# Performance work log

Hardware: AMD Instinct MI355X
Metric: run time of the kernel (lower is better)

## Reference

```python
import jax, jax.numpy as jnp
import numpy as np

B, T, D, H = 2, 2048, 1024, 16
HD = D // H
SCALE = HD ** -0.5
NEG_INF = float(np.finfo(np.float32).min)


def setup_inputs() -> dict:
    key = jax.random.key(0)
    ks = jax.random.split(key, 10)
    s = 1.0 / np.sqrt(D)
    x = jax.random.normal(ks[0], (B, T, D), dtype=jnp.float32)
    # causal mask, True = keep, shape (B,1,T,T)
    mask = jnp.broadcast_to(jnp.tril(jnp.ones((T, T), dtype=bool)), (B, 1, T, T))
    Wq = jax.random.normal(ks[1], (D, D), dtype=jnp.float32) * s
    bq = jax.random.normal(ks[2], (D,), dtype=jnp.float32) * s
    Wk = jax.random.normal(ks[3], (D, D), dtype=jnp.float32) * s
    bk = jax.random.normal(ks[4], (D,), dtype=jnp.float32) * s
    Wv = jax.random.normal(ks[5], (D, D), dtype=jnp.float32) * s
    bv = jax.random.normal(ks[6], (D,), dtype=jnp.float32) * s
    Wo = jax.random.normal(ks[7], (D, D), dtype=jnp.float32) * s
    bo = jax.random.normal(ks[8], (D,), dtype=jnp.float32) * s
    return {"x": x, "mask": mask, "Wq": Wq, "bq": bq, "Wk": Wk, "bk": bk,
            "Wv": Wv, "bv": bv, "Wo": Wo, "bo": bo}


def _split_heads(t):
    # (B,T,D) -> (B,H,T,HD)
    return t.reshape(B, T, H, HD).transpose(0, 2, 1, 3)


def masked_rowwise_softmax(scores, mask):
    # mask: bool, True = keep; fully-masked rows return zeros.
    s = scores.astype(jnp.float32)
    masked = jnp.where(mask, s, NEG_INF)
    row_max = jnp.max(masked, axis=-1, keepdims=True)
    exps = jnp.exp(masked - row_max) * mask.astype(jnp.float32)
    denom = jnp.maximum(jnp.sum(exps, axis=-1, keepdims=True), 1e-12)
    return (exps / denom).astype(scores.dtype)


def reference(x, mask, Wq, bq, Wk, bk, Wv, bv, Wo, bo):
    q = _split_heads(x @ Wq.T + bq)
    k = _split_heads(x @ Wk.T + bk)
    v = _split_heads(x @ Wv.T + bv)
    scores = jnp.einsum('bhqd,bhkd->bhqk', q, k) * SCALE
    m = jnp.broadcast_to(mask, (B, H, T, T))
    attn = masked_rowwise_softmax(scores, m)
    y = jnp.einsum('bhqk,bhkd->bhqd', attn, v)
    y = y.transpose(0, 2, 1, 3).reshape(B, T, D)
    return y @ Wo.T + bo
```

## Files before the change

### kernel.cpp

```cpp
#include <hip/hip_runtime.h>

#define B_ 2
#define H_ 16
#define T_ 2048
#define D_ 1024
#define HD_ 64
#define NEG_HUGE (-3.402823466e38f)
#define QSCALE 0.18033688011112042f

typedef unsigned short u16;
typedef unsigned int u32;
typedef __attribute__((ext_vector_type(8))) short bf16x8;
typedef __attribute__((ext_vector_type(4))) float f32x4;
typedef __attribute__((ext_vector_type(4))) u32 u32x4;

typedef const __attribute__((address_space(1))) void* gas_t;
typedef __attribute__((address_space(3))) void* las_t;

__device__ __forceinline__ u16 f2bf(float f) {
    u32 u = __builtin_bit_cast(u32, f);
    u += 0x7FFFu + ((u >> 16) & 1u);
    return (u16)(u >> 16);
}

__device__ __forceinline__ u32 pk2bf(float f0, float f1) {
    const u32 a0 = __builtin_bit_cast(u32, f0) + 0x8000u;
    const u32 a1 = __builtin_bit_cast(u32, f1) + 0x8000u;
    return __builtin_amdgcn_perm(a1, a0, 0x07060302u);
}

__device__ __forceinline__ uint2 pk4bf(f32x4 a) {
    uint2 r;
    r.x = pk2bf(a[0], a[1]);
    r.y = pk2bf(a[2], a[3]);
    return r;
}

__device__ __forceinline__ f32x4 mfma16(bf16x8 a, bf16x8 b, f32x4 c) {
    return __builtin_amdgcn_mfma_f32_16x16x32_bf16(a, b, c, 0, 0, 0);
}

__global__ __launch_bounds__(256) void to_bf16(
    const float* __restrict__ x,  const float* __restrict__ wq,
    const float* __restrict__ wk, const float* __restrict__ wv,
    const float* __restrict__ wo, u16* __restrict__ dst)
{
    const size_t g = ((size_t)blockIdx.x * 256 + threadIdx.x) * 8;
    const float* src; size_t off;
    if      (g < (size_t)(4u << 20)) { src = x;  off = g; }
    else if (g < (size_t)(5u << 20)) { src = wq; off = g - (size_t)(4u << 20); }
    else if (g < (size_t)(6u << 20)) { src = wk; off = g - (size_t)(5u << 20); }
    else if (g < (size_t)(7u << 20)) { src = wv; off = g - (size_t)(6u << 20); }
    else                             { src = wo; off = g - (size_t)(7u << 20); }
    const float4 a = *(const float4*)&src[off];
    const float4 b = *(const float4*)&src[off + 4];
    ushort4 lo = make_ushort4(f2bf(a.x), f2bf(a.y), f2bf(a.z), f2bf(a.w));
    ushort4 hi = make_ushort4(f2bf(b.x), f2bf(b.y), f2bf(b.z), f2bf(b.w));
    *(ushort4*)&dst[g]     = lo;
    *(ushort4*)&dst[g + 4] = hi;
}

__device__ __forceinline__ void gemm128_core(
    const u16* __restrict__ P0, const u16* __restrict__ P1,
    const int m0, const int n0, u16* As, u16* Bs, f32x4 (&acc)[4][4])
{
    const int tid  = threadIdx.x;
    const int lane = tid & 63;
    const int quad = lane >> 4;
    const int l15  = lane & 15;
    const int w    = tid >> 6;
    const int wm   = (w >> 1) << 6;
    const int wn   = (w & 1) << 6;
    const int swz  = l15 & 7;

    size_t aoff[4], boff[4];
    int    loff[4];
#pragma unroll
    for (int i = 0; i < 4; ++i) {
        const int slot = i * 256 + tid;
        const int r = slot >> 3, c = slot & 7;
        const int gc = (c ^ (r & 7)) << 3;
        aoff[i] = (size_t)(m0 + r) * D_ + gc;
        boff[i] = (size_t)(n0 + r) * D_ + gc;
        loff[i] = slot * 8;
    }
    int rowA[4], rowB[4];
#pragma unroll
    for (int i = 0; i < 4; ++i) {
        rowA[i] = (wm + i * 16 + l15) * 64;
        rowB[i] = (wn + i * 16 + l15) * 64;
    }

    bf16x8 pa[4], pb[4];
#pragma unroll
    for (int i = 0; i < 4; ++i) {
        pa[i] = *(const bf16x8*)&P0[aoff[i]];
        pb[i] = *(const bf16x8*)&P1[boff[i]];
    }

    for (int k0 = 0; k0 < D_; k0 += 64) {
        __syncthreads();
#pragma unroll
        for (int i = 0; i < 4; ++i) {
            *(bf16x8*)&As[loff[i]] = pa[i];
            *(bf16x8*)&Bs[loff[i]] = pb[i];
        }
        if (k0 + 64 < D_) {
            const int kn = k0 + 64;
#pragma unroll
            for (int i = 0; i < 4; ++i) {
                pa[i] = *(const bf16x8*)&P0[aoff[i] + kn];
                pb[i] = *(const bf16x8*)&P1[boff[i] + kn];
            }
        }
        __syncthreads();
#pragma unroll
        for (int s = 0; s < 2; ++s) {
            const int ch = (((s << 2) + quad) ^ swz) << 3;
            bf16x8 am[4], bm[4];
#pragma unroll
            for (int mi = 0; mi < 4; ++mi) am[mi] = *(const bf16x8*)&As[rowA[mi] + ch];
#pragma unroll
            for (int ni = 0; ni < 4; ++ni) bm[ni] = *(const bf16x8*)&Bs[rowB[ni] + ch];
#pragma unroll
            for (int mi = 0; mi < 4; ++mi)
#pragma unroll
                for (int ni = 0; ni < 4; ++ni)
                    acc[mi][ni] = mfma16(am[mi], bm[ni], acc[mi][ni]);
        }
    }
}

__global__ __launch_bounds__(512, 2) void gemm_qkv(
    const u16* __restrict__ xb,
    const u16* __restrict__ Wqb, const u16* __restrict__ Wkb, const u16* __restrict__ Wvb,
    const float* __restrict__ bq, const float* __restrict__ bk, const float* __restrict__ bv,
    u16* __restrict__ Qb, u16* __restrict__ Kb, u16* __restrict__ Vtb)
{
    __shared__ u16 lds[65536];
    const int tid  = threadIdx.x;
    const int lane = tid & 63;
    const int quad = lane >> 4;
    const int l15  = lane & 15;
    const int w    = tid >> 6;
    const int wr   = w >> 2;
    const int wc   = w & 3;
    const int swz7 = l15 & 7;

    const int L  = blockIdx.x;
    const int wg = (L & 7) * 24 + (L >> 3);
    const int ftile = wg >> 4;
    const int ttile = wg & 15;
    const int z  = ftile >> 2;
    const int fb = (ftile & 3) << 8;

    const u16* PA; const u16* PB;
    int Ra, Rb;
    if (z == 0)      { PA = Wqb; PB = xb;  Ra = fb;         Rb = ttile << 8; }
    else if (z == 1) { PA = Wkb; PB = xb;  Ra = fb;         Rb = ttile << 8; }
    else             { PA = xb;  PB = Wvb; Ra = ttile << 8; Rb = fb;         }

    const int rr  = tid >> 3;
    const int cc8 = ((tid & 7) ^ (rr & 7)) << 3;
    size_t srcA[4], srcB[4];
#pragma unroll
    for (int i = 0; i < 4; ++i) {
        srcA[i] = (size_t)(Ra + i * 64 + rr) * D_ + cc8;
        srcB[i] = (size_t)(Rb + i * 64 + rr) * D_ + cc8;
    }
    const int dstT = tid * 8;

#define QKV_STAGE(p, kt) do {                                               \
    const size_t ko_ = (size_t)(kt) * 64;                                   \
    _Pragma("unroll")                                                       \
    for (int i_ = 0; i_ < 4; ++i_)                                          \
        __builtin_amdgcn_global_load_lds((gas_t)(PA + srcA[i_] + ko_),      \
            (las_t)&lds[((p) << 14) + i_ * 4096 + dstT], 16, 0, 0);         \
    _Pragma("unroll")                                                       \
    for (int i_ = 0; i_ < 4; ++i_)                                          \
        __builtin_amdgcn_global_load_lds((gas_t)(PB + srcB[i_] + ko_),      \
            (las_t)&lds[32768 + ((p) << 14) + i_ * 4096 + dstT], 16, 0, 0); \
} while (0)

    const int baseA = ((wr << 7) + l15) * 64;
    const int baseB = 32768 + ((wc << 6) + l15) * 64;
    const int cs0 = (quad ^ swz7) << 3;
    const int cs1 = ((quad + 4) ^ swz7) << 3;

    f32x4 acc[8][4];
#pragma unroll
    for (int i = 0; i < 8; ++i)
#pragma unroll
        for (int j = 0; j < 4; ++j) acc[i][j] = (f32x4){0.f, 0.f, 0.f, 0.f};

    QKV_STAGE(0, 0);
    QKV_STAGE(1, 1);
    asm volatile("s_waitcnt vmcnt(8)" ::: "memory");
    __builtin_amdgcn_s_barrier();

    for (int kt = 0; kt < 16; ++kt) {
        const int pO = (kt & 1) << 14;
        bf16x8 bfr[4][2], afr[4][2];
#pragma unroll
        for (int ni = 0; ni < 4; ++ni) {
            bfr[ni][0] = *(const bf16x8*)&lds[pO + baseB + ni * 1024 + cs0];
            bfr[ni][1] = *(const bf16x8*)&lds[pO + baseB + ni * 1024 + cs1];
        }
#pragma unroll
        for (int mi = 0; mi < 4; ++mi) {
            afr[mi][0] = *(const bf16x8*)&lds[pO + baseA + mi * 1024 + cs0];
            afr[mi][1] = *(const bf16x8*)&lds[pO + baseA + mi * 1024 + cs1];
        }
        __builtin_amdgcn_s_setprio(1);
#pragma unroll
        for (int mi = 0; mi < 4; ++mi)
#pragma unroll
            for (int ni = 0; ni < 4; ++ni) {
                acc[mi][ni] = mfma16(afr[mi][0], bfr[ni][0], acc[mi][ni]);
                acc[mi][ni] = mfma16(afr[mi][1], bfr[ni][1], acc[mi][ni]);
            }
        __builtin_amdgcn_s_setprio(0);
#pragma unroll
        for (int mi = 0; mi < 4; ++mi) {
            afr[mi][0] = *(const bf16x8*)&lds[pO + baseA + (mi + 4) * 1024 + cs0];
            afr[mi][1] = *(const bf16x8*)&lds[pO + baseA + (mi + 4) * 1024 + cs1];
        }
        asm volatile("s_waitcnt lgkmcnt(0)" ::: "memory");
        __builtin_amdgcn_sched_barrier(0);
        __builtin_amdgcn_s_barrier();
        __builtin_amdgcn_sched_barrier(0);
        if (kt + 2 < 16) QKV_STAGE(kt & 1, kt + 2);
        __builtin_amdgcn_s_setprio(1);
#pragma unroll
        for (int mi = 0; mi < 4; ++mi)
#pragma unroll
            for (int ni = 0; ni < 4; ++ni) {
                acc[mi + 4][ni] = mfma16(afr[mi][0], bfr[ni][0], acc[mi + 4][ni]);
                acc[mi + 4][ni] = mfma16(afr[mi][1], bfr[ni][1], acc[mi + 4][ni]);
            }
        __builtin_amdgcn_s_setprio(0);
        if (kt < 14) asm volatile("s_waitcnt vmcnt(8)" ::: "memory");
        else         asm volatile("s_waitcnt vmcnt(0)" ::: "memory");
        __builtin_amdgcn_sched_barrier(0);
        __builtin_amdgcn_s_barrier();
    }
#undef QKV_STAGE

    __syncthreads();
    u16* scr = &lds[w * 8192];
    const int pq   = quad >> 1;
    const int psub = (quad & 1) << 2;

    if (z < 2) {
        const float* bias = (z == 0) ? bq : bk;
        const float  CF   = (z == 0) ? QSCALE : 1.f;
        u16*         Cq   = (z == 0) ? Qb : Kb;
        const int fbw = fb + (wr << 7);
        const int tbw = (ttile << 8) + (wc << 6);
#pragma unroll
        for (int mi = 0; mi < 8; ++mi) {
            const float4 bi = *(const float4*)&bias[fbw + mi * 16 + (quad << 2)];
            const int c = (mi << 1) + pq;
#pragma unroll
            for (int ni = 0; ni < 4; ++ni) {
                const int tl = ni * 16 + l15;
                f32x4 a = acc[mi][ni];
                f32x4 v = { (a[0] + bi.x) * CF, (a[1] + bi.y) * CF,
                            (a[2] + bi.z) * CF, (a[3] + bi.w) * CF };
                *(uint2*)&scr[tl * 128 + ((c ^ (tl & 15)) << 3) + psub] = pk4bf(v);
            }
        }
        __asm__ volatile("s_waitcnt lgkmcnt(0)" ::: "memory");
        const int hb = fbw >> 6;
#pragma unroll
        for (int e = 0; e < 16; ++e) {
            const int tl = (e << 2) + (lane >> 4);
            const int c  = lane & 15;
            bf16x8 v = *(const bf16x8*)&scr[tl * 128 + ((c ^ (tl & 15)) << 3)];
            const int tg = tbw + tl;
            const int bb = tg >> 11, t0 = tg & 2047;
            *(bf16x8*)&Cq[((size_t)((bb << 4) + hb + (c >> 3)) * T_ + t0) * HD_ +
                          ((c & 7) << 3)] = v;
        }
    } else {
        const int fvw = fb + (wc << 6);
        const int h   = fvw >> 6;
        const int tbw = (ttile << 8) + (wr << 7);
#pragma unroll
        for (int ni = 0; ni < 4; ++ni) {
            const int hdrow = ni * 16 + l15;
            const float bi = bv[fvw + ni * 16 + l15];
            const int sw = hdrow & 15;
#pragma unroll
            for (int mi = 0; mi < 8; ++mi) {
                f32x4 a = acc[mi][ni];
                f32x4 v = { a[0] + bi, a[1] + bi, a[2] + bi, a[3] + bi };
                const int c = (mi << 1) + pq;
                *(uint2*)&scr[hdrow * 128 + ((c ^ sw) << 3) + psub] = pk4bf(v);
            }
        }
        __asm__ volatile("s_waitcnt lgkmcnt(0)" ::: "memory");
#pragma unroll
        for (int e = 0; e < 16; ++e) {
            const int hdl = (e << 2) + (lane >> 4);
            const int c   = lane & 15;
            bf16x8 v = *(const bf16x8*)&scr[hdl * 128 + ((c ^ (hdl & 15)) << 3)];
            const int tg = tbw + (c << 3);
            const int bb = tg >> 11, t0 = tg & 2047;
            *(bf16x8*)&Vtb[((size_t)((bb << 4) + h) * HD_ + hdl) * T_ + t0] = v;
        }
    }
}

__global__ __launch_bounds__(256) void gemm_out(
    const u16* __restrict__ Ab, const u16* __restrict__ Wob,
    const float* __restrict__ bo, float* __restrict__ C)
{
    __shared__ u16 As[128 * 64];
    __shared__ u16 Bs[128 * 64];
    const int L   = blockIdx.x;
    const int xcd = L & 7;
    const int kk  = L >> 3;
    const int tt  = (xcd << 2) + (kk & 3);
    const int ft  = kk >> 2;
    const int m0  = tt << 7;
    const int n0  = ft << 7;

    f32x4 acc[4][4];
#pragma unroll
    for (int i = 0; i < 4; ++i)
#pragma unroll
        for (int j = 0; j < 4; ++j) acc[i][j] = (f32x4){0.f, 0.f, 0.f, 0.f};

    gemm128_core(Ab, Wob, m0, n0, As, Bs, acc);

    const int tid  = threadIdx.x;
    const int lane = tid & 63;
    const int quad = lane >> 4;
    const int l15  = lane & 15;
    const int w    = tid >> 6;
    const int wm   = (w >> 1) << 6;
    const int wn   = (w & 1) << 6;

    float bi[4];
#pragma unroll
    for (int ni = 0; ni < 4; ++ni) bi[ni] = bo[n0 + wn + ni * 16 + l15];

#pragma unroll
    for (int mi = 0; mi < 4; ++mi) {
        const int m = m0 + wm + mi * 16 + (quad << 2);
#pragma unroll
        for (int r = 0; r < 4; ++r)
#pragma unroll
            for (int ni = 0; ni < 4; ++ni)
                C[(size_t)(m + r) * D_ + n0 + wn + ni * 16 + l15] = acc[mi][ni][r] + bi[ni];
    }
}

__global__ __launch_bounds__(256) void attn_mfma(
    const u16* __restrict__ Qg, const u16* __restrict__ Kg,
    const u16* __restrict__ Vtg, u16* __restrict__ Out)
{
    __shared__ u16 Ks[128 * 64];
    __shared__ u16 Vs[64 * 128];
    const int tid  = threadIdx.x;
    const int w    = tid >> 6;
    const int lane = tid & 63;
    const int quad = lane >> 4;
    const int l15  = lane & 15;
    const int bh   = blockIdx.x;
    const int qt   = 31 - (int)blockIdx.y;
    const size_t base = (size_t)bh * (T_ * HD_);

    int lK[4], lV[4];
    size_t gK[4], gV[4];
#pragma unroll
    for (int i = 0; i < 4; ++i) {
        const int slot = i * 256 + tid;
        const int rk = slot >> 3, ck = slot & 7;
        lK[i] = rk * 64 + ((ck ^ (rk & 7)) << 3);
        gK[i] = base + (size_t)rk * HD_ + ck * 8;
        const int rv = slot >> 4, cv = slot & 15;
        lV[i] = rv * 128 + ((cv ^ (rv & 15)) << 3);
        gV[i] = base + (size_t)rv * T_ + cv * 8;
    }

    bf16x8 ones;
#pragma unroll
    for (int i = 0; i < 8; ++i) ones[i] = (short)0x3F80;

    const int swz7 = l15 & 7;
    const int b = bh >> 4, h = bh & 15;

    const int qloc = (w << 4) + l15;
    const int qrow = (qt << 6) + qloc;
    const bf16x8 qf0 = *(const bf16x8*)&Qg[base + (size_t)qrow * HD_ + quad * 8];
    const bf16x8 qf1 = *(const bf16x8*)&Qg[base + (size_t)qrow * HD_ + 32 + quad * 8];

    f32x4 o[4];
#pragma unroll
    for (int nt = 0; nt < 4; ++nt) o[nt] = (f32x4){0.f, 0.f, 0.f, 0.f};
    f32x4 Lacc = (f32x4){0.f, 0.f, 0.f, 0.f};

    const int nIter = (qt + 2) >> 1;
    bf16x8 kreg[4], vreg[4];
#pragma unroll
    for (int i = 0; i < 4; ++i) {
        kreg[i] = *(const bf16x8*)&Kg[gK[i]];
        vreg[i] = *(const bf16x8*)&Vtg[gV[i]];
    }

    for (int it = 0; it < nIter; ++it) {
        __syncthreads();
#pragma unroll
        for (int i = 0; i < 4; ++i) {
            *(bf16x8*)&Ks[lK[i]] = kreg[i];
            *(bf16x8*)&Vs[lV[i]] = vreg[i];
        }
        if (it + 1 < nIter) {
            const int koff = (it + 1) << 7;
#pragma unroll
            for (int i = 0; i < 4; ++i) {
                kreg[i] = *(const bf16x8*)&Kg[gK[i] + (size_t)koff * HD_];
                vreg[i] = *(const bf16x8*)&Vtg[gV[i] + koff];
            }
        }
        __syncthreads();

        f32x4 st[8];
#pragma unroll
        for (int t = 0; t < 8; ++t) {
            const int kr = (t * 16 + l15) * 64;
            const bf16x8 k0 = *(const bf16x8*)&Ks[kr + ((quad ^ swz7) << 3)];
            const bf16x8 k1 = *(const bf16x8*)&Ks[kr + (((quad + 4) ^ swz7) << 3)];
            f32x4 a = (f32x4){0.f, 0.f, 0.f, 0.f};
            a = mfma16(k0, qf0, a);
            a = mfma16(k1, qf1, a);
            st[t] = a;
        }

        if (it == nIter - 1) {
            const int koff = it << 7;
#pragma unroll
            for (int t = 0; t < 8; ++t)
#pragma unroll
                for (int r = 0; r < 4; ++r) {
                    const int kg = koff + t * 16 + (quad << 2) + r;
                    if (kg > qrow) st[t][r] = NEG_HUGE;
                }
        }

#pragma unroll
        for (int t = 0; t < 8; ++t)
#pragma unroll
            for (int r = 0; r < 4; ++r) st[t][r] = __builtin_amdgcn_exp2f(st[t][r]);

        bf16x8 pf[4];
#pragma unroll
        for (int kq = 0; kq < 4; ++kq) {
            u32 c00 = pk2bf(st[2 * kq][0],     st[2 * kq][1]);
            u32 c01 = pk2bf(st[2 * kq][2],     st[2 * kq][3]);
            u32 c10 = pk2bf(st[2 * kq + 1][0], st[2 * kq + 1][1]);
            u32 c11 = pk2bf(st[2 * kq + 1][2], st[2 * kq + 1][3]);
            asm("v_permlane32_swap_b32 %0, %1" : "+v"(c00), "+v"(c10));
            asm("v_permlane16_swap_b32 %0, %1" : "+v"(c00), "+v"(c10));
            asm("v_permlane32_swap_b32 %0, %1" : "+v"(c01), "+v"(c11));
            asm("v_permlane16_swap_b32 %0, %1" : "+v"(c01), "+v"(c11));
            u32x4 dw;
            dw[0] = c00; dw[1] = c01; dw[2] = c10; dw[3] = c11;
            pf[kq] = __builtin_bit_cast(bf16x8, dw);
        }

        __builtin_amdgcn_s_setprio(1);
#pragma unroll
        for (int nt = 0; nt < 4; ++nt) {
            f32x4 oo = o[nt];
            const int vr = (nt * 16 + l15) * 128;
#pragma unroll
            for (int kq = 0; kq < 4; ++kq) {
                const bf16x8 vf = *(const bf16x8*)&Vs[vr + ((((kq << 2) + quad) ^ l15) << 3)];
                oo = mfma16(pf[kq], vf, oo);
            }
            o[nt] = oo;
        }
#pragma unroll
        for (int kq = 0; kq < 4; ++kq)
            Lacc = mfma16(pf[kq], ones, Lacc);
        __builtin_amdgcn_s_setprio(0);
    }

    f32x4 linv;
#pragma unroll
    for (int r = 0; r < 4; ++r) linv[r] = 1.f / fmaxf(Lacc[r], 1e-30f);

#pragma unroll
    for (int nt = 0; nt < 4; ++nt)
#pragma unroll
        for (int r = 0; r < 4; ++r) {
            const int qg2 = (qt << 6) + (w << 4) + (quad << 2) + r;
            const u32 u = __builtin_bit_cast(u32, o[nt][r] * linv[r]) + 0x8000u;
            Out[(size_t)(b * T_ + qg2) * D_ + (h << 6) + nt * 16 + l15] = (u16)(u >> 16);
        }
}

extern "C" void kernel_launch(void* const* d_in, const int* in_sizes, int n_in,
                              void* d_out, int out_size, void* d_ws, size_t ws_size,
                              hipStream_t stream)
{
    const float* x  = (const float*)d_in[0];
    const float* Wq = (const float*)d_in[2];
    const float* bq = (const float*)d_in[3];
    const float* Wk = (const float*)d_in[4];
    const float* bk = (const float*)d_in[5];
    const float* Wv = (const float*)d_in[6];
    const float* bv = (const float*)d_in[7];
    const float* Wo = (const float*)d_in[8];
    const float* bo = (const float*)d_in[9];
    float* out = (float*)d_out;

    const size_t M1 = (size_t)1 << 20;
    u16* wsu = (u16*)d_ws;
    u16* xb  = wsu;
    u16* wqb = wsu + 4 * M1;
    u16* wkb = wsu + 5 * M1;
    u16* wvb = wsu + 6 * M1;
    u16* wob = wsu + 7 * M1;
    u16* Qb  = wsu + 8 * M1;
    u16* Kb  = wsu + 12 * M1;
    u16* Vtb = wsu + 16 * M1;
    u16* AOb = wsu + 20 * M1;

    to_bf16<<<4096, 256, 0, stream>>>(x, Wq, Wk, Wv, Wo, wsu);

    gemm_qkv<<<192, 512, 0, stream>>>(xb, wqb, wkb, wvb, bq, bk, bv, Qb, Kb, Vtb);

    dim3 ga(B_ * H_, T_ / 64);
    attn_mfma<<<ga, 256, 0, stream>>>(Qb, Kb, Vtb, AOb);

    gemm_out<<<256, 256, 0, stream>>>(AOb, wob, bo, out);
}
```

Measured before the change: 186.2 us.

## Double-buffer LDS in output GEMM and attention with async global-to-LDS loads

The output projection GEMM drops the shared register-staged core for a two-stage LDS pipeline. It fills LDS with global_load_lds direct copies issued two k-tiles ahead, and splits each k-tile's MFMAs around the barrier with raised wave priority. The attention kernel also double-buffers its K/V tiles in LDS, which cuts the per-iteration barriers from two to one and writes the prefetched tile after compute. The goal is to hide global-load latency and barrier stalls, at the cost of more LDS per block, which may reduce occupancy.

After: 191.1 us. 1.03x slower.

```diff
diff --git a/kernel.cpp b/kernel.cpp
--- a/kernel.cpp
+++ b/kernel.cpp
@@ -60,77 +60,6 @@
     *(ushort4*)&dst[g + 4] = hi;
 }
 
-__device__ __forceinline__ void gemm128_core(
-    const u16* __restrict__ P0, const u16* __restrict__ P1,
-    const int m0, const int n0, u16* As, u16* Bs, f32x4 (&acc)[4][4])
-{
-    const int tid  = threadIdx.x;
-    const int lane = tid & 63;
-    const int quad = lane >> 4;
-    const int l15  = lane & 15;
-    const int w    = tid >> 6;
-    const int wm   = (w >> 1) << 6;
-    const int wn   = (w & 1) << 6;
-    const int swz  = l15 & 7;
-
-    size_t aoff[4], boff[4];
-    int    loff[4];
-#pragma unroll
-    for (int i = 0; i < 4; ++i) {
-        const int slot = i * 256 + tid;
-        const int r = slot >> 3, c = slot & 7;
-        const int gc = (c ^ (r & 7)) << 3;
-        aoff[i] = (size_t)(m0 + r) * D_ + gc;
-        boff[i] = (size_t)(n0 + r) * D_ + gc;
-        loff[i] = slot * 8;
-    }
-    int rowA[4], rowB[4];
-#pragma unroll
-    for (int i = 0; i < 4; ++i) {
-        rowA[i] = (wm + i * 16 + l15) * 64;
-        rowB[i] = (wn + i * 16 + l15) * 64;
-    }
-
-    bf16x8 pa[4], pb[4];
-#pragma unroll
-    for (int i = 0; i < 4; ++i) {
-        pa[i] = *(const bf16x8*)&P0[aoff[i]];
-        pb[i] = *(const bf16x8*)&P1[boff[i]];
-    }
-
-    for (int k0 = 0; k0 < D_; k0 += 64) {
-        __syncthreads();
-#pragma unroll
-        for (int i = 0; i < 4; ++i) {
-            *(bf16x8*)&As[loff[i]] = pa[i];
-            *(bf16x8*)&Bs[loff[i]] = pb[i];
-        }
-        if (k0 + 64 < D_) {
-            const int kn = k0 + 64;
-#pragma unroll
-            for (int i = 0; i < 4; ++i) {
-                pa[i] = *(const bf16x8*)&P0[aoff[i] + kn];
-                pb[i] = *(const bf16x8*)&P1[boff[i] + kn];
-            }
-        }
-        __syncthreads();
-#pragma unroll
-        for (int s = 0; s < 2; ++s) {
-            const int ch = (((s << 2) + quad) ^ swz) << 3;
-            bf16x8 am[4], bm[4];
-#pragma unroll
-            for (int mi = 0; mi < 4; ++mi) am[mi] = *(const bf16x8*)&As[rowA[mi] + ch];
-#pragma unroll
-            for (int ni = 0; ni < 4; ++ni) bm[ni] = *(const bf16x8*)&Bs[rowB[ni] + ch];
-#pragma unroll
-            for (int mi = 0; mi < 4; ++mi)
-#pragma unroll
-                for (int ni = 0; ni < 4; ++ni)
-                    acc[mi][ni] = mfma16(am[mi], bm[ni], acc[mi][ni]);
-        }
-    }
-}
-
 __global__ __launch_bounds__(512, 2) void gemm_qkv(
     const u16* __restrict__ xb,
     const u16* __restrict__ Wqb, const u16* __restrict__ Wkb, const u16* __restrict__ Wvb,
@@ -312,12 +241,20 @@
     }
 }
 
-__global__ __launch_bounds__(256) void gemm_out(
+__global__ __launch_bounds__(256, 1) void gemm_out(
     const u16* __restrict__ Ab, const u16* __restrict__ Wob,
     const float* __restrict__ bo, float* __restrict__ C)
 {
-    __shared__ u16 As[128 * 64];
-    __shared__ u16 Bs[128 * 64];
+    __shared__ u16 lds[32768];
+    const int tid  = threadIdx.x;
+    const int lane = tid & 63;
+    const int quad = lane >> 4;
+    const int l15  = lane & 15;
+    const int w    = tid >> 6;
+    const int wm   = (w >> 1) << 6;
+    const int wn   = (w & 1) << 6;
+    const int swz7 = l15 & 7;
+
     const int L   = blockIdx.x;
     const int xcd = L & 7;
     const int kk  = L >> 3;
@@ -326,21 +263,83 @@
     const int m0  = tt << 7;
     const int n0  = ft << 7;
 
+    const int rr  = tid >> 3;
+    const int cc8 = ((tid & 7) ^ (rr & 7)) << 3;
+    size_t srcA[4], srcB[4];
+#pragma unroll
+    for (int i = 0; i < 4; ++i) {
+        srcA[i] = (size_t)(m0 + i * 32 + rr) * D_ + cc8;
+        srcB[i] = (size_t)(n0 + i * 32 + rr) * D_ + cc8;
+    }
+    const int dstT = tid * 8;
+
+#define OUT_STAGE(p, kt) do {                                               \
+    const size_t ko_ = (size_t)(kt) * 64;                                   \
+    _Pragma("unroll")                                                       \
+    for (int i_ = 0; i_ < 4; ++i_)                                          \
+        __builtin_amdgcn_global_load_lds((gas_t)(Ab + srcA[i_] + ko_),      \
+            (las_t)&lds[((p) << 13) + i_ * 2048 + dstT], 16, 0, 0);         \
+    _Pragma("unroll")                                                       \
+    for (int i_ = 0; i_ < 4; ++i_)                                          \
+        __builtin_amdgcn_global_load_lds((gas_t)(Wob + srcB[i_] + ko_),     \
+            (las_t)&lds[16384 + ((p) << 13) + i_ * 2048 + dstT], 16, 0, 0); \
+} while (0)
+
+    const int baseA = (wm + l15) * 64;
+    const int baseB = 16384 + (wn + l15) * 64;
+    const int cs0 = (quad ^ swz7) << 3;
+    const int cs1 = ((quad + 4) ^ swz7) << 3;
+
     f32x4 acc[4][4];
 #pragma unroll
     for (int i = 0; i < 4; ++i)
 #pragma unroll
         for (int j = 0; j < 4; ++j) acc[i][j] = (f32x4){0.f, 0.f, 0.f, 0.f};
 
-    gemm128_core(Ab, Wob, m0, n0, As, Bs, acc);
-
-    const int tid  = threadIdx.x;
-    const int lane = tid & 63;
-    const int quad = lane >> 4;
-    const int l15  = lane & 15;
-    const int w    = tid >> 6;
-    const int wm   = (w >> 1) << 6;
-    const int wn   = (w & 1) << 6;
+    OUT_STAGE(0, 0);
+    OUT_STAGE(1, 1);
+    asm volatile("s_waitcnt vmcnt(8)" ::: "memory");
+    __builtin_amdgcn_s_barrier();
+
+    for (int kt = 0; kt < 16; ++kt) {
+        const int pO = (kt & 1) << 13;
+        bf16x8 am[4][2], bm[4][2];
+#pragma unroll
+        for (int ni = 0; ni < 4; ++ni) {
+            bm[ni][0] = *(const bf16x8*)&lds[pO + baseB + ni * 1024 + cs0];
+            bm[ni][1] = *(const bf16x8*)&lds[pO + baseB + ni * 1024 + cs1];
+        }
+#pragma unroll
+        for (int mi = 0; mi < 4; ++mi)
+            am[mi][0] = *(const bf16x8*)&lds[pO + baseA + mi * 1024 + cs0];
+        __builtin_amdgcn_s_setprio(1);
+#pragma unroll
+        for (int mi = 0; mi < 4; ++mi)
+#pragma unroll
+            for (int ni = 0; ni < 4; ++ni)
+                acc[mi][ni] = mfma16(am[mi][0], bm[ni][0], acc[mi][ni]);
+        __builtin_amdgcn_s_setprio(0);
+#pragma unroll
+        for (int mi = 0; mi < 4; ++mi)
+            am[mi][1] = *(const bf16x8*)&lds[pO + baseA + mi * 1024 + cs1];
+        asm volatile("s_waitcnt lgkmcnt(0)" ::: "memory");
+        __builtin_amdgcn_sched_barrier(0);
+        __builtin_amdgcn_s_barrier();
+        __builtin_amdgcn_sched_barrier(0);
+        if (kt + 2 < 16) OUT_STAGE(kt & 1, kt + 2);
+        __builtin_amdgcn_s_setprio(1);
+#pragma unroll
+        for (int mi = 0; mi < 4; ++mi)
+#pragma unroll
+            for (int ni = 0; ni < 4; ++ni)
+                acc[mi][ni] = mfma16(am[mi][1], bm[ni][1], acc[mi][ni]);
+        __builtin_amdgcn_s_setprio(0);
+        if (kt < 14) asm volatile("s_waitcnt vmcnt(8)" ::: "memory");
+        else         asm volatile("s_waitcnt vmcnt(0)" ::: "memory");
+        __builtin_amdgcn_sched_barrier(0);
+        __builtin_amdgcn_s_barrier();
+    }
+#undef OUT_STAGE
 
     float bi[4];
 #pragma unroll
@@ -361,8 +360,8 @@
     const u16* __restrict__ Qg, const u16* __restrict__ Kg,
     const u16* __restrict__ Vtg, u16* __restrict__ Out)
 {
-    __shared__ u16 Ks[128 * 64];
-    __shared__ u16 Vs[64 * 128];
+    __shared__ u16 Ks[2][128 * 64];
+    __shared__ u16 Vs[2][64 * 128];
     const int tid  = threadIdx.x;
     const int w    = tid >> 6;
     const int lane = tid & 63;
@@ -409,15 +408,17 @@
         kreg[i] = *(const bf16x8*)&Kg[gK[i]];
         vreg[i] = *(const bf16x8*)&Vtg[gV[i]];
     }
+#pragma unroll
+    for (int i = 0; i < 4; ++i) {
+        *(bf16x8*)&Ks[0][lK[i]] = kreg[i];
+        *(bf16x8*)&Vs[0][lV[i]] = vreg[i];
+    }
+    __syncthreads();
 
     for (int it = 0; it < nIter; ++it) {
-        __syncthreads();
-#pragma unroll
-        for (int i = 0; i < 4; ++i) {
-            *(bf16x8*)&Ks[lK[i]] = kreg[i];
-            *(bf16x8*)&Vs[lV[i]] = vreg[i];
-        }
-        if (it + 1 < nIter) {
+        const int cur = it & 1;
+        const bool pfch = (it + 1 < nIter);
+        if (pfch) {
             const int koff = (it + 1) << 7;
 #pragma unroll
             for (int i = 0; i < 4; ++i) {
@@ -425,14 +426,15 @@
                 vreg[i] = *(const bf16x8*)&Vtg[gV[i] + koff];
             }
         }
-        __syncthreads();
+        const u16* Kc = Ks[cur];
+        const u16* Vc = Vs[cur];
 
         f32x4 st[8];
 #pragma unroll
         for (int t = 0; t < 8; ++t) {
             const int kr = (t * 16 + l15) * 64;
-            const bf16x8 k0 = *(const bf16x8*)&Ks[kr + ((quad ^ swz7) << 3)];
-            const bf16x8 k1 = *(const bf16x8*)&Ks[kr + (((quad + 4) ^ swz7) << 3)];
+            const bf16x8 k0 = *(const bf16x8*)&Kc[kr + ((quad ^ swz7) << 3)];
+            const bf16x8 k1 = *(const bf16x8*)&Kc[kr + (((quad + 4) ^ swz7) << 3)];
             f32x4 a = (f32x4){0.f, 0.f, 0.f, 0.f};
             a = mfma16(k0, qf0, a);
             a = mfma16(k1, qf1, a);
@@ -478,7 +480,7 @@
             const int vr = (nt * 16 + l15) * 128;
 #pragma unroll
             for (int kq = 0; kq < 4; ++kq) {
-                const bf16x8 vf = *(const bf16x8*)&Vs[vr + ((((kq << 2) + quad) ^ l15) << 3)];
+                const bf16x8 vf = *(const bf16x8*)&Vc[vr + ((((kq << 2) + quad) ^ l15) << 3)];
                 oo = mfma16(pf[kq], vf, oo);
             }
             o[nt] = oo;
@@ -487,6 +489,15 @@
         for (int kq = 0; kq < 4; ++kq)
             Lacc = mfma16(pf[kq], ones, Lacc);
         __builtin_amdgcn_s_setprio(0);
+
+        if (pfch) {
+#pragma unroll
+            for (int i = 0; i < 4; ++i) {
+                *(bf16x8*)&Ks[cur ^ 1][lK[i]] = kreg[i];
+                *(bf16x8*)&Vs[cur ^ 1][lV[i]] = vreg[i];
+            }
+        }
+        __syncthreads();
     }
 
     f32x4 linv;
```
